# Optimization experiments

Hardware: AMD Instinct MI355X
Metric: run time of the kernel (lower is better)

## Reference

```python
import jax, jax.numpy as jnp
import numpy as np

B, C, Q, H = 16, 1024, 128, 768  # batch, context_len, query_len, hidden (= proj_size)


def setup_inputs() -> dict:
    key = jax.random.key(0)
    ks = jax.random.split(key, 8)
    s = 1.0 / np.sqrt(H)
    return {
        "context": jax.random.normal(ks[0], (B, C, H), jnp.float32),
        "context_masks": jnp.ones((B, C), jnp.float32),
        "query": jax.random.normal(ks[1], (B, Q, H), jnp.float32),
        "query_masks": jnp.ones((B, Q), jnp.float32),
        "Wc": jax.random.uniform(ks[2], (H, H), jnp.float32, -s, s),   # proj_ctx weight [out,in]
        "bc": jax.random.uniform(ks[3], (H,), jnp.float32, -s, s),
        "Wq": jax.random.uniform(ks[4], (H, H), jnp.float32, -s, s),   # proj_ques weight
        "bq": jax.random.uniform(ks[5], (H,), jnp.float32, -s, s),
        "w_att": jax.random.uniform(ks[6], (H,), jnp.float32, -s, s),  # attention Linear(H,1) weight
        "b_att": jax.random.uniform(ks[7], (), jnp.float32, -s, s),
    }


def reference(context, context_masks, query, query_masks, Wc, bc, Wq, bq, w_att, b_att):
    # Projections (dropout rate = 0 -> identity)
    ctx = jnp.einsum("bch,ph->bcp", context, Wc) + bc          # [B,C,H]
    qry = jnp.einsum("bqh,ph->bqp", query, Wq) + bq            # [B,Q,H]

    # sim[b,c,q] = sum_p w_att[p]*ctx[b,c,p]*qry[b,q,p] + b_att
    # (algebraic collapse of repeat + elementwise-mul + Linear(H,1))
    sim = jnp.einsum("bcp,bqp->bcq", ctx * w_att, qry) + b_att  # [B,C,Q]

    alpha = jax.nn.softmax(sim, axis=-1)
    alpha = alpha * context_masks[:, :, None] * query_masks[:, None, :]
    a = jnp.einsum("bcq,bqp->bcp", alpha, qry)                  # [B,C,H]

    q2c = jnp.max(sim, axis=-1)                                 # [B,C]
    beta = jax.nn.softmax(q2c, axis=-1) * context_masks         # [B,C]
    b = jnp.einsum("bc,bcp->bp", beta, ctx)                     # [B,H]

    c = ctx * a
    d = ctx * b[:, None, :]
    return jnp.concatenate([ctx, a, c, d], axis=-1)             # [B,C,4H]
```

## Files before the change

kernel.cpp:

```cpp
#include <hip/hip_runtime.h>
#include <cstdint>

#define B_ 16
#define C_ 1024
#define Q_ 128
#define H_ 768
#define OSTR (4 * H_)

typedef __attribute__((ext_vector_type(8))) short bf16x8;
typedef __attribute__((ext_vector_type(4))) float f32x4;
typedef __attribute__((ext_vector_type(4))) int int4v;

__device__ __forceinline__ unsigned short f2bf(float x) {
  union { float f; unsigned u; } v; v.f = x;
  unsigned r = v.u + 0x7FFFu + ((v.u >> 16) & 1u);
  return (unsigned short)(r >> 16);
}
__device__ __forceinline__ unsigned pk2(float a, float b) {
  return (unsigned)f2bf(a) | ((unsigned)f2bf(b) << 16);
}
__device__ __forceinline__ float bf2f(unsigned short u) {
  union { unsigned u; float f; } t; t.u = ((unsigned)u) << 16; return t.f;
}

__global__ __launch_bounds__(256) void f2bf4_kernel(
    const float* __restrict__ s0, unsigned short* __restrict__ d0, int n0,
    const float* __restrict__ s1, unsigned short* __restrict__ d1, int n1,
    const float* __restrict__ s2, unsigned short* __restrict__ d2, int n2,
    const float* __restrict__ s3, unsigned short* __restrict__ d3, int n3) {
  int i = blockIdx.x * 256 + threadIdx.x;
  const float* s;
  unsigned short* d;
  if (i < n0) { s = s0; d = d0; }
  else if ((i -= n0) < n1) { s = s1; d = d1; }
  else if ((i -= n1) < n2) { s = s2; d = d2; }
  else if ((i -= n2) < n3) { s = s3; d = d3; }
  else return;
  float4 a = ((const float4*)s)[2 * i];
  float4 b = ((const float4*)s)[2 * i + 1];
  int4v o;
  o[0] = (int)pk2(a.x, a.y); o[1] = (int)pk2(a.z, a.w);
  o[2] = (int)pk2(b.x, b.y); o[3] = (int)pk2(b.z, b.w);
  ((int4v*)d)[i] = o;
}

template <int MODE>
__global__ __launch_bounds__(256) void gemm_uni(
    const unsigned short* __restrict__ A, const unsigned short* __restrict__ Bm,
    const float* __restrict__ bias, unsigned short* __restrict__ ob1,
    unsigned short* __restrict__ ob2, const float* __restrict__ watt,
    const float* __restrict__ cmask, const float* __restrict__ qmask,
    float* __restrict__ q2c, int K, int qchunk) {
  __shared__ __align__(16) unsigned char smem[(MODE == 0) ? 33792 : 16384];
  __shared__ float pmS[2][64];
  __shared__ float psS[2][64];
  constexpr int AROWS = (MODE < 2) ? 128 : 64;
  constexpr int MI = (MODE < 2) ? 4 : 2;
  unsigned short* As = (unsigned short*)smem;
  unsigned short* Ws = (unsigned short*)(smem + ((MODE < 2) ? 8192 : 4096));
  const int tid = threadIdx.x;
  const int lane = tid & 63;
  const int w = tid >> 6;
  const int orig = ((int)blockIdx.x & 7) * qchunk + ((int)blockIdx.x >> 3);
  const int wrA = (w >> 1) * (AROWS / 2);
  const int wcB = (w & 1) * 64;
  const int fr = lane & 15;
  const int fq = lane >> 4;

  int gm, gn, bb;
  const unsigned short *Ap, *Bp;
  if constexpr (MODE == 0 || MODE == 1) {
    gm = (orig / 6) * 128; gn = (orig % 6) * 128; bb = 0;
    Ap = A + (size_t)gm * K; Bp = Bm + (size_t)gn * K;
  } else {
    bb = orig >> 4; gm = bb * C_ + (orig & 15) * 64; gn = 0;
    Ap = A + (size_t)gm * K; Bp = Bm + (size_t)bb * Q_ * K;
  }

  auto stage128 = [&](const unsigned short* __restrict__ G, unsigned short* S, int k0) {
#pragma unroll
    for (int r = 0; r < 2; ++r) {
      const int c = r * 256 + tid;
      const int row = c >> 2, sub = c & 3;
      const unsigned short* g = G + (size_t)row * K + k0 + sub * 8;
      unsigned short* l = S + (size_t)(r * 256 + w * 64) * 8;
      __builtin_amdgcn_global_load_lds(
          (const __attribute__((address_space(1))) void*)g,
          (__attribute__((address_space(3))) void*)l, 16, 0, 0);
    }
  };
  auto stage64 = [&](const unsigned short* __restrict__ G, unsigned short* S, int k0) {
    const int c = tid;
    const int row = c >> 2, sub = c & 3;
    const unsigned short* g = G + (size_t)row * K + k0 + sub * 8;
    unsigned short* l = S + (size_t)(w * 64) * 8;
    __builtin_amdgcn_global_load_lds(
        (const __attribute__((address_space(1))) void*)g,
        (__attribute__((address_space(3))) void*)l, 16, 0, 0);
  };

  f32x4 acc[MI][4];
#pragma unroll
  for (int i = 0; i < MI; ++i)
#pragma unroll
    for (int j = 0; j < 4; ++j)
#pragma unroll
      for (int e = 0; e < 4; ++e) acc[i][j][e] = 0.f;

  for (int k0 = 0; k0 < K; k0 += 32) {
    if constexpr (MODE < 2) stage128(Ap, As, k0); else stage64(Ap, As, k0);
    stage128(Bp, Ws, k0);
    __syncthreads();
    bf16x8 af[MI], wf[4];
#pragma unroll
    for (int i = 0; i < MI; ++i)
      af[i] = *(const bf16x8*)(As + (wrA + i * 16 + fr) * 32 + fq * 8);
#pragma unroll
    for (int j = 0; j < 4; ++j)
      wf[j] = *(const bf16x8*)(Ws + (wcB + j * 16 + fr) * 32 + fq * 8);
#pragma unroll
    for (int i = 0; i < MI; ++i)
#pragma unroll
      for (int j = 0; j < 4; ++j)
        acc[i][j] = __builtin_amdgcn_mfma_f32_16x16x32_bf16(af[i], wf[j], acc[i][j], 0, 0, 0);
    __syncthreads();
  }

  if constexpr (MODE == 0) {
    unsigned short* tr16 = (unsigned short*)smem;
    float bj[4];
#pragma unroll
    for (int j = 0; j < 4; ++j) bj[j] = bias[gn + wcB + j * 16 + fr];
#pragma unroll
    for (int i = 0; i < 4; ++i)
#pragma unroll
      for (int j = 0; j < 4; ++j)
#pragma unroll
        for (int r = 0; r < 4; ++r)
          tr16[(wrA + i * 16 + fq * 4 + r) * 132 + wcB + j * 16 + fr] =
              f2bf(acc[i][j][r] + bj[j]);
    __syncthreads();
#pragma unroll
    for (int k = 0; k < 8; ++k) {
      const int f = k * 256 + tid;
      const int row = f >> 4, c8 = (f & 15) << 3;
      int4v v = *(const int4v*)&tr16[row * 132 + c8];
      *(int4v*)&ob1[(size_t)(gm + row) * H_ + gn + c8] = v;
    }
  } else if constexpr (MODE == 1) {
#pragma unroll
    for (int i = 0; i < 4; ++i) {
#pragma unroll
      for (int j = 0; j < 4; ++j) {
        const int n = gn + wcB + j * 16 + fr;
        const float bias_n = bias[n];
        const float wv = watt[n];
        ushort4 t4;
#pragma unroll
        for (int r = 0; r < 4; ++r) {
          const size_t m = (size_t)gm + wrA + i * 16 + fq * 4 + r;
          float v = acc[i][j][r] + bias_n;
          ob1[m * H_ + n] = f2bf(v * wv);
          (&t4.x)[r] = f2bf(v);
        }
        const int bidx = gm >> 7;
        const int q0 = wrA + i * 16 + fq * 4;
        *(ushort4*)(ob2 + ((size_t)bidx * H_ + n) * Q_ + q0) = t4;
      }
    }
  } else {
    float red[MI][4];
#pragma unroll
    for (int i = 0; i < MI; ++i)
#pragma unroll
      for (int r = 0; r < 4; ++r) {
        float mx = acc[i][0][r];
#pragma unroll
        for (int j = 1; j < 4; ++j) mx = fmaxf(mx, acc[i][j][r]);
        mx = fmaxf(mx, __shfl_xor(mx, 1));
        mx = fmaxf(mx, __shfl_xor(mx, 2));
        mx = fmaxf(mx, __shfl_xor(mx, 4));
        mx = fmaxf(mx, __shfl_xor(mx, 8));
        if (fr == 0) pmS[w & 1][wrA + i * 16 + fq * 4 + r] = mx;
      }
    __syncthreads();
    float qm[4];
#pragma unroll
    for (int j = 0; j < 4; ++j) qm[j] = qmask[bb * Q_ + wcB + j * 16 + fr];
#pragma unroll
    for (int i = 0; i < MI; ++i)
#pragma unroll
      for (int r = 0; r < 4; ++r) {
        const int lr = wrA + i * 16 + fq * 4 + r;
        const float M = fmaxf(pmS[0][lr], pmS[1][lr]);
        if ((w & 1) == 0 && fr == 0) q2c[gm + lr] = M;
        float s = 0.f;
#pragma unroll
        for (int j = 0; j < 4; ++j) {
          acc[i][j][r] = __expf(acc[i][j][r] - M);
          s += acc[i][j][r];
        }
        s += __shfl_xor(s, 1); s += __shfl_xor(s, 2);
        s += __shfl_xor(s, 4); s += __shfl_xor(s, 8);
        if (fr == 0) psS[w & 1][lr] = s;
      }
    __syncthreads();
#pragma unroll
    for (int i = 0; i < MI; ++i)
#pragma unroll
      for (int r = 0; r < 4; ++r) {
        const int lr = wrA + i * 16 + fq * 4 + r;
        const float S = psS[0][lr] + psS[1][lr];
        const float inv = cmask[gm + lr] / S;
#pragma unroll
        for (int j = 0; j < 4; ++j) {
          const int lc = wcB + j * 16 + fr;
          ob1[(size_t)(gm + lr) * Q_ + lc] = f2bf(acc[i][j][r] * inv * qm[j]);
        }
      }
  }
}

__global__ __launch_bounds__(256) void pv_kernel(
    const unsigned short* __restrict__ alpha, const unsigned short* __restrict__ qryT,
    const unsigned short* __restrict__ ctxp, const float* __restrict__ bvec,
    float* __restrict__ out32) {
  __shared__ __align__(16) unsigned char smem[33792];
  const int tid = threadIdx.x;
  const int lane = tid & 63;
  const int w = tid >> 6;
  const int fr = lane & 15;
  const int fq = lane >> 4;
  const int orig = ((int)blockIdx.x & 7) * 192 + ((int)blockIdx.x >> 3);
  const int bb = orig / 96;
  const int rem = orig % 96;
  const int gm = bb * C_ + (rem / 6) * 64;
  const int gn = (rem % 6) * 128;
  const unsigned short* Ap = alpha + (size_t)gm * Q_;
  const unsigned short* Bp = qryT + ((size_t)bb * H_ + gn) * Q_;
  const int wrA = (w >> 1) * 32;
  const int wcB = (w & 1) * 64;
  unsigned short* Ws = (unsigned short*)smem;

#pragma unroll
  for (int kk = 0; kk < 4; ++kk) {
#pragma unroll
    for (int r = 0; r < 2; ++r) {
      const int c = r * 256 + tid;
      const int row = c >> 2, sub = c & 3;
      const unsigned short* g = Bp + (size_t)row * Q_ + kk * 32 + sub * 8;
      unsigned short* l = Ws + kk * 4096 + (size_t)(r * 256 + w * 64) * 8;
      __builtin_amdgcn_global_load_lds(
          (const __attribute__((address_space(1))) void*)g,
          (__attribute__((address_space(3))) void*)l, 16, 0, 0);
    }
  }
  ushort4 cxr[8];
#pragma unroll
  for (int k = 0; k < 8; ++k) {
    const int f = k * 256 + tid;
    const int row = f >> 5, c4 = (f & 31) << 2;
    cxr[k] = *(const ushort4*)&ctxp[(size_t)(gm + row) * H_ + gn + c4];
  }
  bf16x8 af[2][4];
#pragma unroll
  for (int i = 0; i < 2; ++i)
#pragma unroll
    for (int kk = 0; kk < 4; ++kk)
      af[i][kk] = *(const bf16x8*)(Ap + (size_t)(wrA + i * 16 + fr) * Q_ + kk * 32 + fq * 8);

  f32x4 acc[2][4];
#pragma unroll
  for (int i = 0; i < 2; ++i)
#pragma unroll
    for (int j = 0; j < 4; ++j)
#pragma unroll
      for (int e = 0; e < 4; ++e) acc[i][j][e] = 0.f;

  __syncthreads();
#pragma unroll
  for (int kk = 0; kk < 4; ++kk) {
    bf16x8 wf[4];
#pragma unroll
    for (int j = 0; j < 4; ++j)
      wf[j] = *(const bf16x8*)(Ws + kk * 4096 + (wcB + j * 16 + fr) * 32 + fq * 8);
#pragma unroll
    for (int i = 0; i < 2; ++i)
#pragma unroll
      for (int j = 0; j < 4; ++j)
        acc[i][j] = __builtin_amdgcn_mfma_f32_16x16x32_bf16(af[i][kk], wf[j], acc[i][j], 0, 0, 0);
  }
  __syncthreads();

  float* tr = (float*)smem;
#pragma unroll
  for (int i = 0; i < 2; ++i)
#pragma unroll
    for (int j = 0; j < 4; ++j)
#pragma unroll
      for (int r = 0; r < 4; ++r)
        tr[(wrA + i * 16 + fq * 4 + r) * 132 + wcB + j * 16 + fr] = acc[i][j][r];
  __syncthreads();
#pragma unroll
  for (int k = 0; k < 8; ++k) {
    const int f = k * 256 + tid;
    const int row = f >> 5, c4 = (f & 31) << 2;
    float4 av = *(const float4*)&tr[row * 132 + c4];
    const ushort4 cu = cxr[k];
    float4 bv = *(const float4*)&bvec[bb * H_ + gn + c4];
    const float cx0 = bf2f(cu.x), cx1 = bf2f(cu.y), cx2 = bf2f(cu.z), cx3 = bf2f(cu.w);
    float* rowp = out32 + (size_t)(gm + row) * OSTR + gn;
    float4 cxv; cxv.x = cx0; cxv.y = cx1; cxv.z = cx2; cxv.w = cx3;
    *(float4*)&rowp[c4] = cxv;
    *(float4*)&rowp[H_ + c4] = av;
    float4 cc;
    cc.x = cx0 * av.x; cc.y = cx1 * av.y; cc.z = cx2 * av.z; cc.w = cx3 * av.w;
    *(float4*)&rowp[2 * H_ + c4] = cc;
    float4 dd;
    dd.x = cx0 * bv.x; dd.y = cx1 * bv.y; dd.z = cx2 * bv.z; dd.w = cx3 * bv.w;
    *(float4*)&rowp[3 * H_ + c4] = dd;
  }
}

__global__ __launch_bounds__(256) void beta_bvec_kernel(
    const unsigned short* __restrict__ ctxp, const float* __restrict__ q2c,
    const float* __restrict__ cmask, float* __restrict__ bvec) {
  __shared__ float sh[C_];
  __shared__ float red[256];
  const int tid = threadIdx.x;
  const int b = blockIdx.x / 12;
  const int p0 = (blockIdx.x % 12) * 64;
  float v[4];
  float lm = -1e30f;
#pragma unroll
  for (int i = 0; i < 4; ++i) {
    v[i] = q2c[b * C_ + i * 256 + tid];
    lm = fmaxf(lm, v[i]);
  }
  red[tid] = lm;
  __syncthreads();
  for (int off = 128; off > 0; off >>= 1) {
    if (tid < off) red[tid] = fmaxf(red[tid], red[tid + off]);
    __syncthreads();
  }
  const float m = red[0];
  __syncthreads();
  float ls = 0.f;
#pragma unroll
  for (int i = 0; i < 4; ++i) {
    float e = __expf(v[i] - m);
    sh[i * 256 + tid] = e * cmask[b * C_ + i * 256 + tid];
    ls += e;
  }
  red[tid] = ls;
  __syncthreads();
  for (int off = 128; off > 0; off >>= 1) {
    if (tid < off) red[tid] += red[tid + off];
    __syncthreads();
  }
  const float denom = red[0];
  const int pp = tid & 63;
  const int cg = tid >> 6;
  const unsigned short* base = ctxp + ((size_t)(b * C_ + cg)) * H_ + p0 + pp;
  float acc = 0.f;
#pragma unroll 4
  for (int c = cg; c < C_; c += 4) {
    acc += sh[c] * bf2f(*base);
    base += (size_t)4 * H_;
  }
  __syncthreads();
  red[tid] = acc;
  __syncthreads();
  if (tid < 64)
    bvec[b * H_ + p0 + tid] =
        (red[tid] + red[tid + 64] + red[tid + 128] + red[tid + 192]) / denom;
}

extern "C" void kernel_launch(void* const* d_in, const int* in_sizes, int n_in,
                              void* d_out, int out_size, void* d_ws, size_t ws_size,
                              hipStream_t stream) {
  const float* context = (const float*)d_in[0];
  const float* cmask   = (const float*)d_in[1];
  const float* query   = (const float*)d_in[2];
  const float* qmask   = (const float*)d_in[3];
  const float* Wc      = (const float*)d_in[4];
  const float* bc      = (const float*)d_in[5];
  const float* Wq      = (const float*)d_in[6];
  const float* bq      = (const float*)d_in[7];
  const float* w_att   = (const float*)d_in[8];
  float* out = (float*)d_out;

  unsigned short* ws_ctxb = (unsigned short*)d_ws;
  unsigned short* ws_qinb = ws_ctxb + (size_t)B_ * C_ * H_;
  unsigned short* ws_Wcb  = ws_qinb + (size_t)B_ * Q_ * H_;
  unsigned short* ws_Wqb  = ws_Wcb + (size_t)H_ * H_;
  unsigned short* ws_qryW = ws_Wqb + (size_t)H_ * H_;
  unsigned short* ws_qryT = ws_qryW + (size_t)B_ * Q_ * H_;
  unsigned short* ws_ctxp = ws_qryT + (size_t)B_ * H_ * Q_;
  float* ws_q2c  = (float*)(ws_ctxp + (size_t)B_ * C_ * H_);
  float* ws_bvec = ws_q2c + (size_t)B_ * C_;
  unsigned short* ws_alpha = ws_qinb;

  {
    const int n0 = B_ * C_ * H_ / 8;
    const int n1 = B_ * Q_ * H_ / 8;
    const int n2 = H_ * H_ / 8;
    const int n3 = n2;
    const int tot = n0 + n1 + n2 + n3;
    f2bf4_kernel<<<(tot + 255) / 256, 256, 0, stream>>>(
        context, ws_ctxb, n0, query, ws_qinb, n1, Wc, ws_Wcb, n2, Wq, ws_Wqb, n3);
  }
  gemm_uni<1><<<96, 256, 0, stream>>>(
      ws_qinb, ws_Wqb, bq, ws_qryW, ws_qryT, w_att,
      nullptr, nullptr, nullptr, H_, 12);
  gemm_uni<0><<<768, 256, 0, stream>>>(
      ws_ctxb, ws_Wcb, bc, ws_ctxp, nullptr, nullptr,
      nullptr, nullptr, nullptr, H_, 96);
  gemm_uni<2><<<256, 256, 0, stream>>>(
      ws_ctxp, ws_qryW, nullptr, ws_alpha, nullptr, nullptr,
      cmask, qmask, ws_q2c, H_, 32);
  beta_bvec_kernel<<<B_ * 12, 256, 0, stream>>>(ws_ctxp, ws_q2c, cmask, ws_bvec);
  pv_kernel<<<1536, 256, 0, stream>>>(ws_alpha, ws_qryT, ws_ctxp, ws_bvec, out);
}
```

Measured before the change: 161.2 us.

## Fuse sim-softmax with alpha@qry GEMM and move d output into beta kernel

Merges the similarity GEMM and softmax with the alpha×query GEMM and output write into one kernel, so alpha stays in shared memory and is never written to and reread from global memory. The d = ctx*b slice is now written by the beta kernel, which drops the bvec buffer. The transposed query is stored with an XOR swizzle to avoid LDS bank conflicts. In exchange, the fused kernel runs only 256 blocks, each looping over six column chunks, so parallelism and latency hiding drop compared with the former 1536-block pv kernel. The beta kernel also makes strided 4-byte scalar stores.

Measured after the change: 173.4 us. +7.6%, slower.

```diff
diff --git a/kernel.cpp b/kernel.cpp
--- a/kernel.cpp
+++ b/kernel.cpp
@@ -45,37 +45,26 @@
 }
 
 template <int MODE>
-__global__ __launch_bounds__(256) void gemm_uni(
+__global__ __launch_bounds__(256) void gemm_proj(
     const unsigned short* __restrict__ A, const unsigned short* __restrict__ Bm,
     const float* __restrict__ bias, unsigned short* __restrict__ ob1,
     unsigned short* __restrict__ ob2, const float* __restrict__ watt,
-    const float* __restrict__ cmask, const float* __restrict__ qmask,
-    float* __restrict__ q2c, int K, int qchunk) {
+    int K, int qchunk) {
   __shared__ __align__(16) unsigned char smem[(MODE == 0) ? 33792 : 16384];
-  __shared__ float pmS[2][64];
-  __shared__ float psS[2][64];
-  constexpr int AROWS = (MODE < 2) ? 128 : 64;
-  constexpr int MI = (MODE < 2) ? 4 : 2;
   unsigned short* As = (unsigned short*)smem;
-  unsigned short* Ws = (unsigned short*)(smem + ((MODE < 2) ? 8192 : 4096));
+  unsigned short* Ws = (unsigned short*)(smem + 8192);
   const int tid = threadIdx.x;
   const int lane = tid & 63;
   const int w = tid >> 6;
   const int orig = ((int)blockIdx.x & 7) * qchunk + ((int)blockIdx.x >> 3);
-  const int wrA = (w >> 1) * (AROWS / 2);
+  const int wrA = (w >> 1) * 64;
   const int wcB = (w & 1) * 64;
   const int fr = lane & 15;
   const int fq = lane >> 4;
-
-  int gm, gn, bb;
-  const unsigned short *Ap, *Bp;
-  if constexpr (MODE == 0 || MODE == 1) {
-    gm = (orig / 6) * 128; gn = (orig % 6) * 128; bb = 0;
-    Ap = A + (size_t)gm * K; Bp = Bm + (size_t)gn * K;
-  } else {
-    bb = orig >> 4; gm = bb * C_ + (orig & 15) * 64; gn = 0;
-    Ap = A + (size_t)gm * K; Bp = Bm + (size_t)bb * Q_ * K;
-  }
+  const int gm = (orig / 6) * 128;
+  const int gn = (orig % 6) * 128;
+  const unsigned short* Ap = A + (size_t)gm * K;
+  const unsigned short* Bp = Bm + (size_t)gn * K;
 
   auto stage128 = [&](const unsigned short* __restrict__ G, unsigned short* S, int k0) {
 #pragma unroll
@@ -89,37 +78,28 @@
           (__attribute__((address_space(3))) void*)l, 16, 0, 0);
     }
   };
-  auto stage64 = [&](const unsigned short* __restrict__ G, unsigned short* S, int k0) {
-    const int c = tid;
-    const int row = c >> 2, sub = c & 3;
-    const unsigned short* g = G + (size_t)row * K + k0 + sub * 8;
-    unsigned short* l = S + (size_t)(w * 64) * 8;
-    __builtin_amdgcn_global_load_lds(
-        (const __attribute__((address_space(1))) void*)g,
-        (__attribute__((address_space(3))) void*)l, 16, 0, 0);
-  };
-
-  f32x4 acc[MI][4];
-#pragma unroll
-  for (int i = 0; i < MI; ++i)
+
+  f32x4 acc[4][4];
+#pragma unroll
+  for (int i = 0; i < 4; ++i)
 #pragma unroll
     for (int j = 0; j < 4; ++j)
 #pragma unroll
       for (int e = 0; e < 4; ++e) acc[i][j][e] = 0.f;
 
   for (int k0 = 0; k0 < K; k0 += 32) {
-    if constexpr (MODE < 2) stage128(Ap, As, k0); else stage64(Ap, As, k0);
+    stage128(Ap, As, k0);
     stage128(Bp, Ws, k0);
     __syncthreads();
-    bf16x8 af[MI], wf[4];
-#pragma unroll
-    for (int i = 0; i < MI; ++i)
+    bf16x8 af[4], wf[4];
+#pragma unroll
+    for (int i = 0; i < 4; ++i)
       af[i] = *(const bf16x8*)(As + (wrA + i * 16 + fr) * 32 + fq * 8);
 #pragma unroll
     for (int j = 0; j < 4; ++j)
       wf[j] = *(const bf16x8*)(Ws + (wcB + j * 16 + fr) * 32 + fq * 8);
 #pragma unroll
-    for (int i = 0; i < MI; ++i)
+    for (int i = 0; i < 4; ++i)
 #pragma unroll
       for (int j = 0; j < 4; ++j)
         acc[i][j] = __builtin_amdgcn_mfma_f32_16x16x32_bf16(af[i], wf[j], acc[i][j], 0, 0, 0);
@@ -147,7 +127,7 @@
       int4v v = *(const int4v*)&tr16[row * 132 + c8];
       *(int4v*)&ob1[(size_t)(gm + row) * H_ + gn + c8] = v;
     }
-  } else if constexpr (MODE == 1) {
+  } else {
 #pragma unroll
     for (int i = 0; i < 4; ++i) {
 #pragma unroll
@@ -165,13 +145,84 @@
         }
         const int bidx = gm >> 7;
         const int q0 = wrA + i * 16 + fq * 4;
-        *(ushort4*)(ob2 + ((size_t)bidx * H_ + n) * Q_ + q0) = t4;
+        const int rc = n & 127;
+        const size_t cbase = ((size_t)bidx * H_ + (n & ~127)) * Q_;
+        const int off = rc * 128 + ((((q0 >> 3) ^ (rc & 7)) << 3) | (q0 & 7));
+        *(ushort4*)(ob2 + cbase + off) = t4;
       }
     }
-  } else {
-    float red[MI][4];
-#pragma unroll
-    for (int i = 0; i < MI; ++i)
+  }
+}
+
+__global__ __launch_bounds__(256) void attn_fused(
+    const unsigned short* __restrict__ ctxp, const unsigned short* __restrict__ qryW,
+    const unsigned short* __restrict__ qryT, const float* __restrict__ cmask,
+    const float* __restrict__ qmask, float* __restrict__ q2c,
+    float* __restrict__ out32) {
+  __shared__ __align__(16) unsigned char S[33792];
+  __shared__ __align__(16) unsigned short P[64 * 132];
+  __shared__ float pmS[2][64];
+  __shared__ float psS[2][64];
+  const int tid = threadIdx.x;
+  const int lane = tid & 63;
+  const int w = tid >> 6;
+  const int fr = lane & 15;
+  const int fq = lane >> 4;
+  const int orig = ((int)blockIdx.x & 7) * 32 + ((int)blockIdx.x >> 3);
+  const int bb = orig >> 4;
+  const int gm = bb * C_ + (orig & 15) * 64;
+  const int wrA = (w >> 1) * 32;
+  const int wcB = (w & 1) * 64;
+  const unsigned short* Ap = ctxp + (size_t)gm * H_;
+  const unsigned short* Bp = qryW + (size_t)bb * Q_ * H_;
+  unsigned short* Su = (unsigned short*)S;
+
+  f32x4 acc[2][4];
+#pragma unroll
+  for (int i = 0; i < 2; ++i)
+#pragma unroll
+    for (int j = 0; j < 4; ++j)
+#pragma unroll
+      for (int e = 0; e < 4; ++e) acc[i][j][e] = 0.f;
+
+  for (int k0 = 0; k0 < H_; k0 += 32) {
+    {
+      const int row = tid >> 2, sub = tid & 3;
+      const unsigned short* g = Ap + (size_t)row * H_ + k0 + sub * 8;
+      unsigned short* l = Su + (size_t)(w * 64) * 8;
+      __builtin_amdgcn_global_load_lds(
+          (const __attribute__((address_space(1))) void*)g,
+          (__attribute__((address_space(3))) void*)l, 16, 0, 0);
+    }
+#pragma unroll
+    for (int r = 0; r < 2; ++r) {
+      const int c = r * 256 + tid;
+      const int row = c >> 2, sub = c & 3;
+      const unsigned short* g = Bp + (size_t)row * H_ + k0 + sub * 8;
+      unsigned short* l = Su + 2048 + (size_t)(r * 256 + w * 64) * 8;
+      __builtin_amdgcn_global_load_lds(
+          (const __attribute__((address_space(1))) void*)g,
+          (__attribute__((address_space(3))) void*)l, 16, 0, 0);
+    }
+    __syncthreads();
+    bf16x8 af[2], wf[4];
+#pragma unroll
+    for (int i = 0; i < 2; ++i)
+      af[i] = *(const bf16x8*)(Su + (wrA + i * 16 + fr) * 32 + fq * 8);
+#pragma unroll
+    for (int j = 0; j < 4; ++j)
+      wf[j] = *(const bf16x8*)(Su + 2048 + (wcB + j * 16 + fr) * 32 + fq * 8);
+#pragma unroll
+    for (int i = 0; i < 2; ++i)
+#pragma unroll
+      for (int j = 0; j < 4; ++j)
+        acc[i][j] = __builtin_amdgcn_mfma_f32_16x16x32_bf16(af[i], wf[j], acc[i][j], 0, 0, 0);
+    __syncthreads();
+  }
+
+  {
+#pragma unroll
+    for (int i = 0; i < 2; ++i)
 #pragma unroll
       for (int r = 0; r < 4; ++r) {
         float mx = acc[i][0][r];
@@ -188,7 +239,7 @@
 #pragma unroll
     for (int j = 0; j < 4; ++j) qm[j] = qmask[bb * Q_ + wcB + j * 16 + fr];
 #pragma unroll
-    for (int i = 0; i < MI; ++i)
+    for (int i = 0; i < 2; ++i)
 #pragma unroll
       for (int r = 0; r < 4; ++r) {
         const int lr = wrA + i * 16 + fq * 4 + r;
@@ -206,127 +257,101 @@
       }
     __syncthreads();
 #pragma unroll
-    for (int i = 0; i < MI; ++i)
+    for (int i = 0; i < 2; ++i)
 #pragma unroll
       for (int r = 0; r < 4; ++r) {
         const int lr = wrA + i * 16 + fq * 4 + r;
-        const float S = psS[0][lr] + psS[1][lr];
-        const float inv = cmask[gm + lr] / S;
-#pragma unroll
-        for (int j = 0; j < 4; ++j) {
-          const int lc = wcB + j * 16 + fr;
-          ob1[(size_t)(gm + lr) * Q_ + lc] = f2bf(acc[i][j][r] * inv * qm[j]);
-        }
+        const float S2 = psS[0][lr] + psS[1][lr];
+        const float inv = cmask[gm + lr] / S2;
+#pragma unroll
+        for (int j = 0; j < 4; ++j)
+          P[lr * 132 + wcB + j * 16 + fr] = f2bf(acc[i][j][r] * inv * qm[j]);
       }
   }
-}
-
-__global__ __launch_bounds__(256) void pv_kernel(
-    const unsigned short* __restrict__ alpha, const unsigned short* __restrict__ qryT,
-    const unsigned short* __restrict__ ctxp, const float* __restrict__ bvec,
-    float* __restrict__ out32) {
-  __shared__ __align__(16) unsigned char smem[33792];
-  const int tid = threadIdx.x;
-  const int lane = tid & 63;
-  const int w = tid >> 6;
-  const int fr = lane & 15;
-  const int fq = lane >> 4;
-  const int orig = ((int)blockIdx.x & 7) * 192 + ((int)blockIdx.x >> 3);
-  const int bb = orig / 96;
-  const int rem = orig % 96;
-  const int gm = bb * C_ + (rem / 6) * 64;
-  const int gn = (rem % 6) * 128;
-  const unsigned short* Ap = alpha + (size_t)gm * Q_;
-  const unsigned short* Bp = qryT + ((size_t)bb * H_ + gn) * Q_;
-  const int wrA = (w >> 1) * 32;
-  const int wcB = (w & 1) * 64;
-  unsigned short* Ws = (unsigned short*)smem;
-
-#pragma unroll
-  for (int kk = 0; kk < 4; ++kk) {
-#pragma unroll
-    for (int r = 0; r < 2; ++r) {
-      const int c = r * 256 + tid;
-      const int row = c >> 2, sub = c & 3;
-      const unsigned short* g = Bp + (size_t)row * Q_ + kk * 32 + sub * 8;
-      unsigned short* l = Ws + kk * 4096 + (size_t)(r * 256 + w * 64) * 8;
+  __syncthreads();
+
+  bf16x8 paf[2][4];
+#pragma unroll
+  for (int i = 0; i < 2; ++i)
+#pragma unroll
+    for (int kk = 0; kk < 4; ++kk)
+      paf[i][kk] = *(const bf16x8*)&P[(wrA + i * 16 + fr) * 132 + kk * 32 + fq * 8];
+
+  const unsigned short* Tb = qryT + (size_t)bb * H_ * Q_;
+  for (int ch = 0; ch < 6; ++ch) {
+    const int gn = ch * 128;
+#pragma unroll
+    for (int it = 0; it < 8; ++it) {
+      const unsigned short* g = Tb + (size_t)gn * Q_ + it * 2048 + tid * 8;
+      unsigned short* l = Su + (size_t)(it * 2048) + (size_t)(w * 64) * 8;
       __builtin_amdgcn_global_load_lds(
           (const __attribute__((address_space(1))) void*)g,
           (__attribute__((address_space(3))) void*)l, 16, 0, 0);
     }
-  }
-  ushort4 cxr[8];
-#pragma unroll
-  for (int k = 0; k < 8; ++k) {
-    const int f = k * 256 + tid;
-    const int row = f >> 5, c4 = (f & 31) << 2;
-    cxr[k] = *(const ushort4*)&ctxp[(size_t)(gm + row) * H_ + gn + c4];
-  }
-  bf16x8 af[2][4];
-#pragma unroll
-  for (int i = 0; i < 2; ++i)
-#pragma unroll
-    for (int kk = 0; kk < 4; ++kk)
-      af[i][kk] = *(const bf16x8*)(Ap + (size_t)(wrA + i * 16 + fr) * Q_ + kk * 32 + fq * 8);
-
-  f32x4 acc[2][4];
-#pragma unroll
-  for (int i = 0; i < 2; ++i)
-#pragma unroll
-    for (int j = 0; j < 4; ++j)
-#pragma unroll
-      for (int e = 0; e < 4; ++e) acc[i][j][e] = 0.f;
-
-  __syncthreads();
-#pragma unroll
-  for (int kk = 0; kk < 4; ++kk) {
-    bf16x8 wf[4];
-#pragma unroll
-    for (int j = 0; j < 4; ++j)
-      wf[j] = *(const bf16x8*)(Ws + kk * 4096 + (wcB + j * 16 + fr) * 32 + fq * 8);
+    ushort4 cxr[8];
+#pragma unroll
+    for (int k = 0; k < 8; ++k) {
+      const int f = k * 256 + tid;
+      const int row = f >> 5, c4 = (f & 31) << 2;
+      cxr[k] = *(const ushort4*)&ctxp[(size_t)(gm + row) * H_ + gn + c4];
+    }
+    __syncthreads();
+    f32x4 pac[2][4];
 #pragma unroll
     for (int i = 0; i < 2; ++i)
 #pragma unroll
       for (int j = 0; j < 4; ++j)
-        acc[i][j] = __builtin_amdgcn_mfma_f32_16x16x32_bf16(af[i][kk], wf[j], acc[i][j], 0, 0, 0);
-  }
-  __syncthreads();
-
-  float* tr = (float*)smem;
-#pragma unroll
-  for (int i = 0; i < 2; ++i)
-#pragma unroll
-    for (int j = 0; j < 4; ++j)
-#pragma unroll
-      for (int r = 0; r < 4; ++r)
-        tr[(wrA + i * 16 + fq * 4 + r) * 132 + wcB + j * 16 + fr] = acc[i][j][r];
-  __syncthreads();
-#pragma unroll
-  for (int k = 0; k < 8; ++k) {
-    const int f = k * 256 + tid;
-    const int row = f >> 5, c4 = (f & 31) << 2;
-    float4 av = *(const float4*)&tr[row * 132 + c4];
-    const ushort4 cu = cxr[k];
-    float4 bv = *(const float4*)&bvec[bb * H_ + gn + c4];
-    const float cx0 = bf2f(cu.x), cx1 = bf2f(cu.y), cx2 = bf2f(cu.z), cx3 = bf2f(cu.w);
-    float* rowp = out32 + (size_t)(gm + row) * OSTR + gn;
-    float4 cxv; cxv.x = cx0; cxv.y = cx1; cxv.z = cx2; cxv.w = cx3;
-    *(float4*)&rowp[c4] = cxv;
-    *(float4*)&rowp[H_ + c4] = av;
-    float4 cc;
-    cc.x = cx0 * av.x; cc.y = cx1 * av.y; cc.z = cx2 * av.z; cc.w = cx3 * av.w;
-    *(float4*)&rowp[2 * H_ + c4] = cc;
-    float4 dd;
-    dd.x = cx0 * bv.x; dd.y = cx1 * bv.y; dd.z = cx2 * bv.z; dd.w = cx3 * bv.w;
-    *(float4*)&rowp[3 * H_ + c4] = dd;
-  }
-}
-
-__global__ __launch_bounds__(256) void beta_bvec_kernel(
+#pragma unroll
+        for (int e = 0; e < 4; ++e) pac[i][j][e] = 0.f;
+#pragma unroll
+    for (int kk = 0; kk < 4; ++kk) {
+      bf16x8 wf[4];
+#pragma unroll
+      for (int j = 0; j < 4; ++j) {
+        const int rp = wcB + j * 16 + fr;
+        wf[j] = *(const bf16x8*)(Su + rp * 128 + (((kk * 4 + fq) ^ (rp & 7)) << 3));
+      }
+#pragma unroll
+      for (int i = 0; i < 2; ++i)
+#pragma unroll
+        for (int j = 0; j < 4; ++j)
+          pac[i][j] = __builtin_amdgcn_mfma_f32_16x16x32_bf16(paf[i][kk], wf[j], pac[i][j], 0, 0, 0);
+    }
+    __syncthreads();
+    float* tr = (float*)S;
+#pragma unroll
+    for (int i = 0; i < 2; ++i)
+#pragma unroll
+      for (int j = 0; j < 4; ++j)
+#pragma unroll
+        for (int r = 0; r < 4; ++r)
+          tr[(wrA + i * 16 + fq * 4 + r) * 132 + wcB + j * 16 + fr] = pac[i][j][r];
+    __syncthreads();
+#pragma unroll
+    for (int k = 0; k < 8; ++k) {
+      const int f = k * 256 + tid;
+      const int row = f >> 5, c4 = (f & 31) << 2;
+      float4 av = *(const float4*)&tr[row * 132 + c4];
+      const ushort4 cu = cxr[k];
+      const float cx0 = bf2f(cu.x), cx1 = bf2f(cu.y), cx2 = bf2f(cu.z), cx3 = bf2f(cu.w);
+      float* rowp = out32 + (size_t)(gm + row) * OSTR + gn;
+      float4 cxv; cxv.x = cx0; cxv.y = cx1; cxv.z = cx2; cxv.w = cx3;
+      *(float4*)&rowp[c4] = cxv;
+      *(float4*)&rowp[H_ + c4] = av;
+      float4 cc;
+      cc.x = cx0 * av.x; cc.y = cx1 * av.y; cc.z = cx2 * av.z; cc.w = cx3 * av.w;
+      *(float4*)&rowp[2 * H_ + c4] = cc;
+    }
+    __syncthreads();
+  }
+}
+
+__global__ __launch_bounds__(256) void beta_d_kernel(
     const unsigned short* __restrict__ ctxp, const float* __restrict__ q2c,
-    const float* __restrict__ cmask, float* __restrict__ bvec) {
+    const float* __restrict__ cmask, float* __restrict__ out32) {
   __shared__ float sh[C_];
   __shared__ float red[256];
+  __shared__ float bb64[64];
   const int tid = threadIdx.x;
   const int b = blockIdx.x / 12;
   const int p0 = (blockIdx.x % 12) * 64;
@@ -372,8 +397,17 @@
   red[tid] = acc;
   __syncthreads();
   if (tid < 64)
-    bvec[b * H_ + p0 + tid] =
-        (red[tid] + red[tid + 64] + red[tid + 128] + red[tid + 192]) / denom;
+    bb64[tid] = (red[tid] + red[tid + 64] + red[tid + 128] + red[tid + 192]) / denom;
+  __syncthreads();
+  const float bv = bb64[pp];
+  float* b2 = out32 + ((size_t)(b * C_ + cg)) * OSTR + 3 * H_ + p0 + pp;
+  const unsigned short* cb = ctxp + ((size_t)(b * C_ + cg)) * H_ + p0 + pp;
+#pragma unroll 4
+  for (int c = cg; c < C_; c += 4) {
+    *b2 = bf2f(*cb) * bv;
+    b2 += (size_t)4 * OSTR;
+    cb += (size_t)4 * H_;
+  }
 }
 
 extern "C" void kernel_launch(void* const* d_in, const int* in_sizes, int n_in,
@@ -397,9 +431,7 @@
   unsigned short* ws_qryW = ws_Wqb + (size_t)H_ * H_;
   unsigned short* ws_qryT = ws_qryW + (size_t)B_ * Q_ * H_;
   unsigned short* ws_ctxp = ws_qryT + (size_t)B_ * H_ * Q_;
-  float* ws_q2c  = (float*)(ws_ctxp + (size_t)B_ * C_ * H_);
-  float* ws_bvec = ws_q2c + (size_t)B_ * C_;
-  unsigned short* ws_alpha = ws_qinb;
+  float* ws_q2c = (float*)(ws_ctxp + (size_t)B_ * C_ * H_);
 
   {
     const int n0 = B_ * C_ * H_ / 8;
@@ -410,15 +442,11 @@
     f2bf4_kernel<<<(tot + 255) / 256, 256, 0, stream>>>(
         context, ws_ctxb, n0, query, ws_qinb, n1, Wc, ws_Wcb, n2, Wq, ws_Wqb, n3);
   }
-  gemm_uni<1><<<96, 256, 0, stream>>>(
-      ws_qinb, ws_Wqb, bq, ws_qryW, ws_qryT, w_att,
-      nullptr, nullptr, nullptr, H_, 12);
-  gemm_uni<0><<<768, 256, 0, stream>>>(
-      ws_ctxb, ws_Wcb, bc, ws_ctxp, nullptr, nullptr,
-      nullptr, nullptr, nullptr, H_, 96);
-  gemm_uni<2><<<256, 256, 0, stream>>>(
-      ws_ctxp, ws_qryW, nullptr, ws_alpha, nullptr, nullptr,
-      cmask, qmask, ws_q2c, H_, 32);
-  beta_bvec_kernel<<<B_ * 12, 256, 0, stream>>>(ws_ctxp, ws_q2c, cmask, ws_bvec);
-  pv_kernel<<<1536, 256, 0, stream>>>(ws_alpha, ws_qryT, ws_ctxp, ws_bvec, out);
-}
+  gemm_proj<1><<<96, 256, 0, stream>>>(
+      ws_qinb, ws_Wqb, bq, ws_qryW, ws_qryT, w_att, H_, 12);
+  gemm_proj<0><<<768, 256, 0, stream>>>(
+      ws_ctxb, ws_Wcb, bc, ws_ctxp, nullptr, nullptr, H_, 96);
+  attn_fused<<<256, 256, 0, stream>>>(
+      ws_ctxp, ws_qryW, ws_qryT, cmask, qmask, ws_q2c, out);
+  beta_d_kernel<<<B_ * 12, 256, 0, stream>>>(ws_ctxp, ws_q2c, cmask, out);
+}
```
